# Optimization experiments

Hardware: AMD Instinct MI355X
Metric: run time of the kernel (lower is better)

## Reference

```python
import jax, jax.numpy as jnp
import numpy as np

N_NODES = 50000


def gcn_conv(x, src, dst, norm, W, b):
    # x: [N, Fin] -> linear transform then normalized scatter-add aggregation
    h = x @ W  # [N, Fout]
    msg = h[src] * norm[:, None]  # [E', Fout] gather + scale
    out = jax.ops.segment_sum(msg, dst, num_segments=N_NODES)  # scatter-add
    return out + b


def _build_graph(edge_index):
    # add self-loops (PyG GCNConv default) and compute symmetric normalization
    n = N_NODES
    loops = jnp.arange(n, dtype=edge_index.dtype)
    src = jnp.concatenate([edge_index[0], loops])
    dst = jnp.concatenate([edge_index[1], loops])
    deg = jax.ops.segment_sum(jnp.ones_like(dst, dtype=jnp.float32), dst, num_segments=n)
    dinv = jnp.where(deg > 0, jax.lax.rsqrt(deg), 0.0)
    norm = dinv[src] * dinv[dst]  # [E+N]
    return src, dst, norm


def setup_inputs() -> dict:
    key = jax.random.key(0)
    ks = jax.random.split(key, 8)
    in_c, out_c = 128, 64
    hid = 2 * out_c
    n_edges = 800000
    x = jax.random.normal(ks[0], (N_NODES, in_c), dtype=jnp.float32)
    edge_index = jax.random.randint(ks[1], (2, n_edges), 0, N_NODES, dtype=jnp.int64)
    s = 1.0 / np.sqrt(in_c)
    W1 = jax.random.uniform(ks[2], (in_c, hid), minval=-s, maxval=s, dtype=jnp.float32)
    b1 = jnp.zeros((hid,), dtype=jnp.float32)
    s2 = 1.0 / np.sqrt(hid)
    W_mu = jax.random.uniform(ks[3], (hid, out_c), minval=-s2, maxval=s2, dtype=jnp.float32)
    b_mu = jnp.zeros((out_c,), dtype=jnp.float32)
    W_ls = jax.random.uniform(ks[4], (hid, out_c), minval=-s2, maxval=s2, dtype=jnp.float32)
    b_ls = jnp.zeros((out_c,), dtype=jnp.float32)
    return {"x": x, "edge_index": edge_index, "W1": W1, "b1": b1,
            "W_mu": W_mu, "b_mu": b_mu, "W_ls": W_ls, "b_ls": b_ls}


def reference(x, edge_index, W1, b1, W_mu, b_mu, W_ls, b_ls):
    src, dst, norm = _build_graph(edge_index)
    h = jax.nn.relu(gcn_conv(x, src, dst, norm, W1, b1))
    mu = gcn_conv(h, src, dst, norm, W_mu, b_mu)
    logstd = gcn_conv(h, src, dst, norm, W_ls, b_ls)
    return mu, logstd
```

## Files before the change

### kernel.cpp

```cpp
#include <hip/hip_runtime.h>

#define N_NODES 50000
#define NE      800000
#define FDIM    128
#define OUTC    64
#define CAP     64
#define NXCD    8
#define SLICE   6250
#define NCHK    391

typedef _Float16 half4 __attribute__((ext_vector_type(4)));
typedef _Float16 f16x8 __attribute__((ext_vector_type(8)));
typedef float    f32x4 __attribute__((ext_vector_type(4)));



__global__ __launch_bounds__(256) void k_prep(int4* __restrict__ deg4,
                                              const float* __restrict__ W1,
                                              const float* __restrict__ Wmu,
                                              const float* __restrict__ Wls,
                                              const float* __restrict__ bmu,
                                              const float* __restrict__ bls,
                                              _Float16* __restrict__ W1T,
                                              _Float16* __restrict__ WoT,
                                              float* __restrict__ bo) {
    int b = blockIdx.x, tid = threadIdx.x;
    if (b < 49) {
        int i = b * 256 + tid;
        if (i < 12500) deg4[i] = make_int4(0, 0, 0, 0);
    } else {
        int j = (b - 49) * 256 + tid;
        if (j < 16384) {
            int n = j >> 7, k = j & 127;
            W1T[j] = (_Float16)W1[k * 128 + n];
        } else if (j < 32768) {
            int jj = j - 16384;
            int n = jj >> 7, k = jj & 127;
            WoT[jj] = (_Float16)(n < 64 ? Wmu[k * 64 + n] : Wls[k * 64 + (n - 64)]);
        } else if (j < 32896) {
            int n = j - 32768;
            bo[n] = (n < 64) ? bmu[n] : bls[n - 64];
        }
    }
}


__global__ __launch_bounds__(256) void k_count_fill(const int* __restrict__ ei,
                                                    int* __restrict__ deg,
                                                    int* __restrict__ pks) {
    int bid = blockIdx.x;
    int k8  = bid & 7;
    int lo  = k8 * SLICE;
    int chunk = bid >> 3;
    int base = chunk * 2048 + threadIdx.x;
    #pragma unroll
    for (int j = 0; j < 8; ++j) {
        int e = base + j * 256;
        if (e < NE) {
            int d = ei[NE + e];
            unsigned int rel = (unsigned int)(d - lo);
            if (rel < SLICE) {
                int s = ei[e];
                int slot = atomicAdd(&deg[d], 1);
                if (slot < CAP) pks[d * CAP + slot] = s;
            }
        }
    }
}


__global__ __launch_bounds__(256) void k_scale(const float* __restrict__ x,
                                               const int* __restrict__ deg,
                                               float* __restrict__ dinv,
                                               _Float16* __restrict__ x16) {
    int i = blockIdx.x * 256 + threadIdx.x;
    if (i >= (N_NODES * FDIM) / 4) return;
    int node = i >> 5;
    float dv = rsqrtf((float)(deg[node] + 1));
    if ((i & 31) == 0) dinv[node] = dv;
    float4 v = reinterpret_cast<const float4*>(x)[i];
    half4 h = {(_Float16)(dv * v.x), (_Float16)(dv * v.y),
               (_Float16)(dv * v.z), (_Float16)(dv * v.w)};
    reinterpret_cast<half4*>(x16)[i] = h;
}


__device__ __forceinline__ void add4h(float4& a, half4 h) {
    a.x += (float)h.x; a.y += (float)h.y; a.z += (float)h.z; a.w += (float)h.w;
}

__device__ __forceinline__ void agg_tile(const _Float16* __restrict__ in,
                                         const int* __restrict__ pks,
                                         const int* __restrict__ deg,
                                         const float* __restrict__ dinv,
                                         _Float16 (*__restrict__ As)[136]) {
    int tid = threadIdx.x;
    int rl = tid >> 5;
    int r  = blockIdx.x * 16 + rl;
    int lane4 = (tid & 31) * 4;
    int cnt = deg[r]; if (cnt > CAP) cnt = CAP;
    const int* prow = pks + r * CAP;
    float4 a0 = {0,0,0,0}, a1 = {0,0,0,0}, a2 = {0,0,0,0}, a3 = {0,0,0,0};
    int e = 0;
    for (; e + 4 <= cnt; e += 4) {
        int s0 = prow[e], s1 = prow[e+1], s2 = prow[e+2], s3 = prow[e+3];
        add4h(a0, *reinterpret_cast<const half4*>(&in[(size_t)s0 * FDIM + lane4]));
        add4h(a1, *reinterpret_cast<const half4*>(&in[(size_t)s1 * FDIM + lane4]));
        add4h(a2, *reinterpret_cast<const half4*>(&in[(size_t)s2 * FDIM + lane4]));
        add4h(a3, *reinterpret_cast<const half4*>(&in[(size_t)s3 * FDIM + lane4]));
    }
    for (; e < cnt; ++e)
        add4h(a0, *reinterpret_cast<const half4*>(&in[(size_t)prow[e] * FDIM + lane4]));
    add4h(a1, *reinterpret_cast<const half4*>(&in[(size_t)r * FDIM + lane4]));
    float dv = dinv[r];
    half4 g = {(_Float16)(dv * ((a0.x + a1.x) + (a2.x + a3.x))),
               (_Float16)(dv * ((a0.y + a1.y) + (a2.y + a3.y))),
               (_Float16)(dv * ((a0.z + a1.z) + (a2.z + a3.z))),
               (_Float16)(dv * ((a0.w + a1.w) + (a2.w + a3.w)))};
    *reinterpret_cast<half4*>(&As[rl][lane4]) = g;
}


__global__ __launch_bounds__(512) void k_layer1(const _Float16* __restrict__ x16,
                                                const int* __restrict__ pks,
                                                const int* __restrict__ deg,
                                                const float* __restrict__ dinv,
                                                const _Float16* __restrict__ W1T,
                                                const float* __restrict__ b1,
                                                _Float16* __restrict__ H16) {
    __shared__ _Float16 As[16][136];
    agg_tile(x16, pks, deg, dinv, As);
    __syncthreads();
    int tid = threadIdx.x;
    int wave = tid >> 6, lane = tid & 63;
    int colg = lane & 15;
    int kg8 = (lane >> 4) * 8;
    f32x4 acc = {0.f, 0.f, 0.f, 0.f};
    #pragma unroll
    for (int ks = 0; ks < 4; ++ks) {
        f16x8 a  = *reinterpret_cast<const f16x8*>(&As[colg][ks * 32 + kg8]);
        f16x8 bf = *reinterpret_cast<const f16x8*>(
            &W1T[(size_t)(wave * 16 + colg) * FDIM + ks * 32 + kg8]);
        acc = __builtin_amdgcn_mfma_f32_16x16x32_f16(a, bf, acc, 0, 0, 0);
    }
    int col = wave * 16 + colg;
    float bias = b1[col];
    int r0 = (lane >> 4) * 4;
    #pragma unroll
    for (int r = 0; r < 4; ++r) {
        int m = blockIdx.x * 16 + r0 + r;
        float h = fmaxf(acc[r] + bias, 0.f);
        H16[(size_t)m * FDIM + col] = (_Float16)(dinv[m] * h);
    }
}

__global__ __launch_bounds__(512) void k_layer2(const _Float16* __restrict__ h16,
                                                const int* __restrict__ pks,
                                                const int* __restrict__ deg,
                                                const float* __restrict__ dinv,
                                                const _Float16* __restrict__ WoT,
                                                const float* __restrict__ bo,
                                                float* __restrict__ MU,
                                                float* __restrict__ LS) {
    __shared__ _Float16 As[16][136];
    agg_tile(h16, pks, deg, dinv, As);
    __syncthreads();
    int tid = threadIdx.x;
    int wave = tid >> 6, lane = tid & 63;
    int colg = lane & 15;
    int kg8 = (lane >> 4) * 8;
    f32x4 acc = {0.f, 0.f, 0.f, 0.f};
    #pragma unroll
    for (int ks = 0; ks < 4; ++ks) {
        f16x8 a  = *reinterpret_cast<const f16x8*>(&As[colg][ks * 32 + kg8]);
        f16x8 bf = *reinterpret_cast<const f16x8*>(
            &WoT[(size_t)(wave * 16 + colg) * FDIM + ks * 32 + kg8]);
        acc = __builtin_amdgcn_mfma_f32_16x16x32_f16(a, bf, acc, 0, 0, 0);
    }
    int col = wave * 16 + colg;
    float bias = bo[col];
    int r0 = (lane >> 4) * 4;
    #pragma unroll
    for (int r = 0; r < 4; ++r) {
        int m = blockIdx.x * 16 + r0 + r;
        float v = acc[r] + bias;
        if (col < 64) MU[(size_t)m * OUTC + col] = v;
        else          LS[(size_t)m * OUTC + (col - 64)] = v;
    }
}


extern "C" void kernel_launch(void* const* d_in, const int* in_sizes, int n_in,
                              void* d_out, int out_size, void* d_ws, size_t ws_size,
                              hipStream_t stream) {
    const float* x   = (const float*)d_in[0];
    const int*   ei  = (const int*)d_in[1];
    const float* W1  = (const float*)d_in[2];
    const float* b1  = (const float*)d_in[3];
    const float* Wmu = (const float*)d_in[4];
    const float* bmu = (const float*)d_in[5];
    const float* Wls = (const float*)d_in[6];
    const float* bls = (const float*)d_in[7];
    float* out = (float*)d_out;

    char* ws = (char*)d_ws;
    int*      deg  = (int*)     (ws + 0);
    float*    dinv = (float*)   (ws + 200000);
    int*      pks  = (int*)     (ws + 400000);
    _Float16* W1T  = (_Float16*)(ws + 13200000);
    _Float16* WoT  = (_Float16*)(ws + 13232768);
    float*    bo   = (float*)   (ws + 13265536);
    _Float16* h16  = (_Float16*)(ws + 13266048);

    _Float16* x16 = (_Float16*)d_out;

    k_prep      <<<49 + 129, 256, 0, stream>>>((int4*)deg, W1, Wmu, Wls, bmu, bls,
                                               W1T, WoT, bo);
    k_count_fill<<<NXCD * NCHK, 256, 0, stream>>>(ei, deg, pks);
    k_scale     <<<(N_NODES * FDIM / 4 + 255) / 256, 256, 0, stream>>>(x, deg, dinv, x16);

    k_layer1<<<N_NODES / 16, 512, 0, stream>>>(x16, pks, deg, dinv, W1T, b1, h16);
    k_layer2<<<N_NODES / 16, 512, 0, stream>>>(h16, pks, deg, dinv, WoT, bo,
                                               out, out + (size_t)N_NODES * OUTC);
}
```

Baseline: 150.3 us.

## Aggregate neighbors directly into MFMA fragments, one wave per row tile

New measurement: 202.8 us. 1.35x slower.

```diff
diff --git a/kernel.cpp b/kernel.cpp
--- a/kernel.cpp
+++ b/kernel.cpp
@@ -8,6 +8,7 @@
 #define NXCD    8
 #define SLICE   6250
 #define NCHK    391
+#define NTILE   3125
 
 typedef _Float16 half4 __attribute__((ext_vector_type(4)));
 typedef _Float16 f16x8 __attribute__((ext_vector_type(8)));
@@ -85,76 +86,100 @@
 }
 
 
-__device__ __forceinline__ void add4h(float4& a, half4 h) {
-    a.x += (float)h.x; a.y += (float)h.y; a.z += (float)h.z; a.w += (float)h.w;
-}
-
-__device__ __forceinline__ void agg_tile(const _Float16* __restrict__ in,
-                                         const int* __restrict__ pks,
-                                         const int* __restrict__ deg,
-                                         const float* __restrict__ dinv,
-                                         _Float16 (*__restrict__ As)[136]) {
-    int tid = threadIdx.x;
-    int rl = tid >> 5;
-    int r  = blockIdx.x * 16 + rl;
-    int lane4 = (tid & 31) * 4;
+__device__ __forceinline__ float agg_frag(const _Float16* __restrict__ in,
+                                          const int* __restrict__ pks,
+                                          const int* __restrict__ deg,
+                                          const float* __restrict__ dinv,
+                                          int r, int p, f16x8* afr) {
     int cnt = deg[r]; if (cnt > CAP) cnt = CAP;
     const int* prow = pks + r * CAP;
-    float4 a0 = {0,0,0,0}, a1 = {0,0,0,0}, a2 = {0,0,0,0}, a3 = {0,0,0,0};
+    float ac0[4][8] = {{0}}, ac1[4][8] = {{0}};
+    const _Float16* base = in + p;
     int e = 0;
-    for (; e + 4 <= cnt; e += 4) {
-        int s0 = prow[e], s1 = prow[e+1], s2 = prow[e+2], s3 = prow[e+3];
-        add4h(a0, *reinterpret_cast<const half4*>(&in[(size_t)s0 * FDIM + lane4]));
-        add4h(a1, *reinterpret_cast<const half4*>(&in[(size_t)s1 * FDIM + lane4]));
-        add4h(a2, *reinterpret_cast<const half4*>(&in[(size_t)s2 * FDIM + lane4]));
-        add4h(a3, *reinterpret_cast<const half4*>(&in[(size_t)s3 * FDIM + lane4]));
-    }
-    for (; e < cnt; ++e)
-        add4h(a0, *reinterpret_cast<const half4*>(&in[(size_t)prow[e] * FDIM + lane4]));
-    add4h(a1, *reinterpret_cast<const half4*>(&in[(size_t)r * FDIM + lane4]));
+    for (; e + 2 <= cnt; e += 2) {
+        int s0 = prow[e], s1 = prow[e + 1];
+        const _Float16* p0 = base + (size_t)s0 * FDIM;
+        const _Float16* p1 = base + (size_t)s1 * FDIM;
+        #pragma unroll
+        for (int ks = 0; ks < 4; ++ks) {
+            f16x8 v0 = *reinterpret_cast<const f16x8*>(p0 + ks * 32);
+            f16x8 v1 = *reinterpret_cast<const f16x8*>(p1 + ks * 32);
+            #pragma unroll
+            for (int j = 0; j < 8; ++j) { ac0[ks][j] += (float)v0[j]; ac1[ks][j] += (float)v1[j]; }
+        }
+    }
+    if (e < cnt) {
+        const _Float16* p0 = base + (size_t)prow[e] * FDIM;
+        #pragma unroll
+        for (int ks = 0; ks < 4; ++ks) {
+            f16x8 v0 = *reinterpret_cast<const f16x8*>(p0 + ks * 32);
+            #pragma unroll
+            for (int j = 0; j < 8; ++j) ac0[ks][j] += (float)v0[j];
+        }
+    }
+    {
+        const _Float16* p0 = base + (size_t)r * FDIM;
+        #pragma unroll
+        for (int ks = 0; ks < 4; ++ks) {
+            f16x8 v0 = *reinterpret_cast<const f16x8*>(p0 + ks * 32);
+            #pragma unroll
+            for (int j = 0; j < 8; ++j) ac1[ks][j] += (float)v0[j];
+        }
+    }
     float dv = dinv[r];
-    half4 g = {(_Float16)(dv * ((a0.x + a1.x) + (a2.x + a3.x))),
-               (_Float16)(dv * ((a0.y + a1.y) + (a2.y + a3.y))),
-               (_Float16)(dv * ((a0.z + a1.z) + (a2.z + a3.z))),
-               (_Float16)(dv * ((a0.w + a1.w) + (a2.w + a3.w)))};
-    *reinterpret_cast<half4*>(&As[rl][lane4]) = g;
-}
-
-
-__global__ __launch_bounds__(512) void k_layer1(const _Float16* __restrict__ x16,
+    #pragma unroll
+    for (int ks = 0; ks < 4; ++ks) {
+        f16x8 g;
+        #pragma unroll
+        for (int j = 0; j < 8; ++j) g[j] = (_Float16)(dv * (ac0[ks][j] + ac1[ks][j]));
+        afr[ks] = g;
+    }
+    return dv;
+}
+
+__global__ __launch_bounds__(256) void k_layer1(const _Float16* __restrict__ x16,
                                                 const int* __restrict__ pks,
                                                 const int* __restrict__ deg,
                                                 const float* __restrict__ dinv,
                                                 const _Float16* __restrict__ W1T,
                                                 const float* __restrict__ b1,
                                                 _Float16* __restrict__ H16) {
-    __shared__ _Float16 As[16][136];
-    agg_tile(x16, pks, deg, dinv, As);
-    __syncthreads();
     int tid = threadIdx.x;
-    int wave = tid >> 6, lane = tid & 63;
-    int colg = lane & 15;
-    int kg8 = (lane >> 4) * 8;
-    f32x4 acc = {0.f, 0.f, 0.f, 0.f};
+    int tile = blockIdx.x * 4 + (tid >> 6);
+    if (tile >= NTILE) return;
+    int lane = tid & 63;
+    int rl = lane & 15;
+    int r  = tile * 16 + rl;
+    int p  = (lane >> 4) * 8;
+    f16x8 afr[4];
+    agg_frag(x16, pks, deg, dinv, r, p, afr);
+    f32x4 acc[8];
+    #pragma unroll
+    for (int t = 0; t < 8; ++t) acc[t] = (f32x4){0.f, 0.f, 0.f, 0.f};
     #pragma unroll
     for (int ks = 0; ks < 4; ++ks) {
-        f16x8 a  = *reinterpret_cast<const f16x8*>(&As[colg][ks * 32 + kg8]);
-        f16x8 bf = *reinterpret_cast<const f16x8*>(
-            &W1T[(size_t)(wave * 16 + colg) * FDIM + ks * 32 + kg8]);
-        acc = __builtin_amdgcn_mfma_f32_16x16x32_f16(a, bf, acc, 0, 0, 0);
-    }
-    int col = wave * 16 + colg;
-    float bias = b1[col];
-    int r0 = (lane >> 4) * 4;
-    #pragma unroll
-    for (int r = 0; r < 4; ++r) {
-        int m = blockIdx.x * 16 + r0 + r;
-        float h = fmaxf(acc[r] + bias, 0.f);
-        H16[(size_t)m * FDIM + col] = (_Float16)(dinv[m] * h);
-    }
-}
-
-__global__ __launch_bounds__(512) void k_layer2(const _Float16* __restrict__ h16,
+        #pragma unroll
+        for (int t = 0; t < 8; ++t) {
+            f16x8 bf = *reinterpret_cast<const f16x8*>(
+                &W1T[(size_t)(t * 16 + rl) * FDIM + ks * 32 + p]);
+            acc[t] = __builtin_amdgcn_mfma_f32_16x16x32_f16(afr[ks], bf, acc[t], 0, 0, 0);
+        }
+    }
+    int m0 = tile * 16 + (lane >> 4) * 4;
+    float dvm[4] = {dinv[m0], dinv[m0 + 1], dinv[m0 + 2], dinv[m0 + 3]};
+    #pragma unroll
+    for (int t = 0; t < 8; ++t) {
+        int col = t * 16 + rl;
+        float bias = b1[col];
+        #pragma unroll
+        for (int rg = 0; rg < 4; ++rg) {
+            float h = fmaxf(acc[t][rg] + bias, 0.f);
+            H16[(size_t)(m0 + rg) * FDIM + col] = (_Float16)(dvm[rg] * h);
+        }
+    }
+}
+
+__global__ __launch_bounds__(256) void k_layer2(const _Float16* __restrict__ h16,
                                                 const int* __restrict__ pks,
                                                 const int* __restrict__ deg,
                                                 const float* __restrict__ dinv,
@@ -162,30 +187,38 @@
                                                 const float* __restrict__ bo,
                                                 float* __restrict__ MU,
                                                 float* __restrict__ LS) {
-    __shared__ _Float16 As[16][136];
-    agg_tile(h16, pks, deg, dinv, As);
-    __syncthreads();
     int tid = threadIdx.x;
-    int wave = tid >> 6, lane = tid & 63;
-    int colg = lane & 15;
-    int kg8 = (lane >> 4) * 8;
-    f32x4 acc = {0.f, 0.f, 0.f, 0.f};
+    int tile = blockIdx.x * 4 + (tid >> 6);
+    if (tile >= NTILE) return;
+    int lane = tid & 63;
+    int rl = lane & 15;
+    int r  = tile * 16 + rl;
+    int p  = (lane >> 4) * 8;
+    f16x8 afr[4];
+    agg_frag(h16, pks, deg, dinv, r, p, afr);
+    f32x4 acc[8];
+    #pragma unroll
+    for (int t = 0; t < 8; ++t) acc[t] = (f32x4){0.f, 0.f, 0.f, 0.f};
     #pragma unroll
     for (int ks = 0; ks < 4; ++ks) {
-        f16x8 a  = *reinterpret_cast<const f16x8*>(&As[colg][ks * 32 + kg8]);
-        f16x8 bf = *reinterpret_cast<const f16x8*>(
-            &WoT[(size_t)(wave * 16 + colg) * FDIM + ks * 32 + kg8]);
-        acc = __builtin_amdgcn_mfma_f32_16x16x32_f16(a, bf, acc, 0, 0, 0);
-    }
-    int col = wave * 16 + colg;
-    float bias = bo[col];
-    int r0 = (lane >> 4) * 4;
-    #pragma unroll
-    for (int r = 0; r < 4; ++r) {
-        int m = blockIdx.x * 16 + r0 + r;
-        float v = acc[r] + bias;
-        if (col < 64) MU[(size_t)m * OUTC + col] = v;
-        else          LS[(size_t)m * OUTC + (col - 64)] = v;
+        #pragma unroll
+        for (int t = 0; t < 8; ++t) {
+            f16x8 bf = *reinterpret_cast<const f16x8*>(
+                &WoT[(size_t)(t * 16 + rl) * FDIM + ks * 32 + p]);
+            acc[t] = __builtin_amdgcn_mfma_f32_16x16x32_f16(afr[ks], bf, acc[t], 0, 0, 0);
+        }
+    }
+    int m0 = tile * 16 + (lane >> 4) * 4;
+    #pragma unroll
+    for (int t = 0; t < 8; ++t) {
+        int col = t * 16 + rl;
+        float bias = bo[col];
+        #pragma unroll
+        for (int rg = 0; rg < 4; ++rg) {
+            float v = acc[t][rg] + bias;
+            if (col < 64) MU[(size_t)(m0 + rg) * OUTC + col] = v;
+            else          LS[(size_t)(m0 + rg) * OUTC + (col - 64)] = v;
+        }
     }
 }
 
@@ -219,7 +252,7 @@
     k_count_fill<<<NXCD * NCHK, 256, 0, stream>>>(ei, deg, pks);
     k_scale     <<<(N_NODES * FDIM / 4 + 255) / 256, 256, 0, stream>>>(x, deg, dinv, x16);
 
-    k_layer1<<<N_NODES / 16, 512, 0, stream>>>(x16, pks, deg, dinv, W1T, b1, h16);
-    k_layer2<<<N_NODES / 16, 512, 0, stream>>>(h16, pks, deg, dinv, WoT, bo,
-                                               out, out + (size_t)N_NODES * OUTC);
-}
+    k_layer1<<<(NTILE + 3) / 4, 256, 0, stream>>>(x16, pks, deg, dinv, W1T, b1, h16);
+    k_layer2<<<(NTILE + 3) / 4, 256, 0, stream>>>(h16, pks, deg, dinv, WoT, bo,
+                                                  out, out + (size_t)N_NODES * OUTC);
+}
```
